# Optimization experiments

Hardware: AMD Instinct MI355X
Metric: run time of the kernel (lower is better)

## Reference

```python
import jax, jax.numpy as jnp
import numpy as np
import math

B, T, DIM, NH = 2, 2048, 2048, 16
HD = DIM // NH  # 128


def rotate_half(x):
    h = x.shape[-1] // 2
    return jnp.concatenate([-x[..., h:], x[..., :h]], axis=-1)


def rope_tables(t_len, rot_dim, base=10000.0, dtype=jnp.float32):
    # rot_dim = head_dim; inv_freq has rot_dim//2 entries -> sin/cos [T, rot_dim//2]
    inv_freq = 1.0 / (base ** (jnp.arange(0, rot_dim, 2, dtype=dtype) / rot_dim))
    t = jnp.arange(t_len, dtype=dtype)
    ang = jnp.einsum('i,j->ij', t, inv_freq)  # [T, rot_dim//2]
    return jnp.sin(ang), jnp.cos(ang)


def apply_rope(q, k, sin, cos):
    # Partial RoPE as in source: rotate only the first half of head_dim,
    # using sin/cos of width head_dim//2 matched to that half.
    h = q.shape[-1] // 2
    q1, q2 = q[..., :h], q[..., h:]
    k1, k2 = k[..., :h], k[..., h:]
    sin = sin[None, None]  # [1,1,T,h]
    cos = cos[None, None]
    q1r = q1 * cos + rotate_half(q1) * sin
    k1r = k1 * cos + rotate_half(k1) * sin
    return jnp.concatenate([q1r, q2], axis=-1), jnp.concatenate([k1r, k2], axis=-1)


def setup_inputs() -> dict:
    key = jax.random.key(0)
    ks = jax.random.split(key, 5)
    s = 1.0 / math.sqrt(DIM)
    return {
        'x': jax.random.normal(ks[0], (B, T, DIM), jnp.float32),
        'wq': jax.random.normal(ks[1], (DIM, DIM), jnp.float32) * s,
        'wk': jax.random.normal(ks[2], (DIM, DIM), jnp.float32) * s,
        'wv': jax.random.normal(ks[3], (DIM, DIM), jnp.float32) * s,
        'wo': jax.random.normal(ks[4], (DIM, DIM), jnp.float32) * s,
    }


def reference(x, wq, wk, wv, wo):
    b, t, c = x.shape
    def proj(w):
        return (x @ w.T).reshape(b, t, NH, HD).transpose(0, 2, 1, 3)  # [B,H,T,hd]
    q, k, v = proj(wq), proj(wk), proj(wv)
    sin, cos = rope_tables(t, HD, dtype=x.dtype)
    q, k = apply_rope(q, k, sin, cos)
    att = jnp.einsum('bhqd,bhkd->bhqk', q, k) * (1.0 / math.sqrt(HD))  # [B,H,T,T]
    att = jax.nn.softmax(att, axis=-1)
    y = jnp.einsum('bhqk,bhkd->bhqd', att, v)
    y = y.transpose(0, 2, 1, 3).reshape(b, t, c)
    return y @ wo.T
```

## Files before the change

kernel.cpp:

```cpp
#include <hip/hip_runtime.h>

typedef unsigned short u16;
typedef __attribute__((ext_vector_type(4))) u16 u16x4;
typedef __attribute__((ext_vector_type(8))) __bf16 bf16x8;
typedef __attribute__((ext_vector_type(4))) float f32x4;

#define B_ 2
#define T_ 2048
#define DIM_ 2048
#define NH_ 16
#define HD_ 128

__device__ __forceinline__ u16 f2b(float f) {
  unsigned u = __builtin_bit_cast(unsigned, f);
  u += 0x7fffu + ((u >> 16) & 1u);
  return (u16)(u >> 16);
}
__device__ __forceinline__ float b2f(u16 h) {
  unsigned u = ((unsigned)h) << 16;
  return __builtin_bit_cast(float, u);
}
__device__ __forceinline__ unsigned pack2(float lo, float hi) {
  return (unsigned)f2b(lo) | ((unsigned)f2b(hi) << 16);
}

typedef __attribute__((address_space(1))) void gvoid_t;
typedef __attribute__((address_space(3))) void lvoid_t;
__device__ __forceinline__ void gload16(const void* g, void* l) {
  __builtin_amdgcn_global_load_lds((gvoid_t*)g, (lvoid_t*)l, 16, 0, 0);
}

__global__ __launch_bounds__(256) void cvt_bf16(const float* x, const float* wq,
    const float* wk, const float* wv, const float* wo,
    u16* xb, u16* wqb, u16* wkb, u16* wvb, u16* wob) {
  int ten = blockIdx.y;
  const float* s; u16* d; int n4;
  if (ten == 0)      { s = x;  d = xb;  n4 = 2097152; }
  else if (ten == 1) { s = wq; d = wqb; n4 = 1048576; }
  else if (ten == 2) { s = wk; d = wkb; n4 = 1048576; }
  else if (ten == 3) { s = wv; d = wvb; n4 = 1048576; }
  else               { s = wo; d = wob; n4 = 1048576; }
  int i = blockIdx.x * 256 + threadIdx.x;
  if (i >= n4) return;
  float4 f = ((const float4*)s)[i];
  u16x4 o = { f2b(f.x), f2b(f.y), f2b(f.z), f2b(f.w) };
  ((u16x4*)d)[i] = o;
}

template <typename OutT>
__device__ __forceinline__ void gemm256_body(const u16* A, const u16* Bw, OutT* C) {
  constexpr int K = 2048, N = 2048;
  __shared__ u16 As[3][256 * 64];
  __shared__ u16 Bs[3][128 * 64];
  const int tid = threadIdx.x;
  const int w = tid >> 6, l = tid & 63, n = l & 15, quad = l >> 4;
  const int wr = w >> 1, wc = w & 1;
  const int row0 = blockIdx.y * 256, col0 = blockIdx.x * 128;

  const u16* aSrc[4];
  const u16* bSrc[2];
#pragma unroll
  for (int i = 0; i < 4; ++i) {
    int ci = i * 512 + tid, r = ci >> 3, cl = ci & 7, cg = cl ^ (r & 7);
    aSrc[i] = A + (size_t)(row0 + r) * K + cg * 8;
  }
#pragma unroll
  for (int i = 0; i < 2; ++i) {
    int ci = i * 512 + tid, r = ci >> 3, cl = ci & 7, cg = cl ^ (r & 7);
    bSrc[i] = Bw + (size_t)(col0 + r) * K + cg * 8;
  }
  const int ldsW = (w * 64) * 16;

  auto stA = [&](int kt, int bufi, int i) {
    gload16(aSrc[i] + kt * 64, (char*)As[bufi] + i * 8192 + ldsW);
  };
  auto stB = [&](int kt, int bufi, int i) {
    gload16(bSrc[i] + kt * 64, (char*)Bs[bufi] + i * 8192 + ldsW);
  };

  const int arow = (wr * 64 + n) * 64;
  const int brow = (wc * 64 + n) * 64;
  const int sw = n & 7;

  f32x4 acc[4][4] = {};

#pragma unroll
  for (int i = 0; i < 4; ++i) stA(0, 0, i);
#pragma unroll
  for (int i = 0; i < 2; ++i) stB(0, 0, i);
#pragma unroll
  for (int i = 0; i < 4; ++i) stA(1, 1, i);
#pragma unroll
  for (int i = 0; i < 2; ++i) stB(1, 1, i);
  asm volatile("s_waitcnt vmcnt(6)" ::: "memory");
  __builtin_amdgcn_s_barrier();

  int buf = 0, nbuf = 2;
#pragma unroll 1
  for (int kt = 0; kt < 32; ++kt) {
    const bool pf = kt < 30;
    const u16* Ab = As[buf];
    const u16* Bb = Bs[buf];
    bf16x8 af[4][2], bfr[2][2];

#pragma unroll
    for (int mt = 0; mt < 4; ++mt)
#pragma unroll
      for (int ks = 0; ks < 2; ++ks)
        af[mt][ks] = *(const bf16x8*)&Ab[arow + mt * 1024 + (((ks * 4 + quad) ^ sw) * 8)];
#pragma unroll
    for (int nt = 0; nt < 2; ++nt)
#pragma unroll
      for (int ks = 0; ks < 2; ++ks)
        bfr[nt][ks] = *(const bf16x8*)&Bb[brow + nt * 1024 + (((ks * 4 + quad) ^ sw) * 8)];
    if (pf) { stA(kt + 2, nbuf, 0); stA(kt + 2, nbuf, 1); stB(kt + 2, nbuf, 0); }
    __builtin_amdgcn_s_barrier();
    asm volatile("s_waitcnt lgkmcnt(0)" ::: "memory");
    __builtin_amdgcn_sched_barrier(0);
    __builtin_amdgcn_s_setprio(1);
#pragma unroll
    for (int ks = 0; ks < 2; ++ks)
#pragma unroll
      for (int mt = 0; mt < 4; ++mt)
#pragma unroll
        for (int nt = 0; nt < 2; ++nt)
          acc[mt][nt] = __builtin_amdgcn_mfma_f32_16x16x32_bf16(af[mt][ks], bfr[nt][ks], acc[mt][nt], 0, 0, 0);
    __builtin_amdgcn_s_setprio(0);
    __builtin_amdgcn_s_barrier();

#pragma unroll
    for (int nt = 0; nt < 2; ++nt)
#pragma unroll
      for (int ks = 0; ks < 2; ++ks)
        bfr[nt][ks] = *(const bf16x8*)&Bb[brow + (nt + 2) * 1024 + (((ks * 4 + quad) ^ sw) * 8)];
    if (pf) { stA(kt + 2, nbuf, 2); stA(kt + 2, nbuf, 3); stB(kt + 2, nbuf, 1); }
    if (pf) asm volatile("s_waitcnt vmcnt(6)" ::: "memory");
    else    asm volatile("s_waitcnt vmcnt(0)" ::: "memory");
    __builtin_amdgcn_s_barrier();
    asm volatile("s_waitcnt lgkmcnt(0)" ::: "memory");
    __builtin_amdgcn_sched_barrier(0);
    __builtin_amdgcn_s_setprio(1);
#pragma unroll
    for (int ks = 0; ks < 2; ++ks)
#pragma unroll
      for (int mt = 0; mt < 4; ++mt)
#pragma unroll
        for (int nt = 0; nt < 2; ++nt)
          acc[mt][nt + 2] = __builtin_amdgcn_mfma_f32_16x16x32_bf16(af[mt][ks], bfr[nt][ks], acc[mt][nt + 2], 0, 0, 0);
    __builtin_amdgcn_s_setprio(0);
    __builtin_amdgcn_s_barrier();

    buf = (buf == 2) ? 0 : buf + 1;
    nbuf = (nbuf == 2) ? 0 : nbuf + 1;
  }

#pragma unroll
  for (int mt = 0; mt < 4; ++mt)
#pragma unroll
    for (int nt = 0; nt < 4; ++nt)
#pragma unroll
      for (int r = 0; r < 4; ++r) {
        size_t idx = (size_t)(row0 + wr * 64 + mt * 16 + quad * 4 + r) * N + (col0 + wc * 64 + nt * 16 + n);
        float v = acc[mt][nt][r];
        if constexpr (sizeof(OutT) == 2) C[idx] = f2b(v); else C[idx] = v;
      }
}

__global__ __launch_bounds__(512, 2) void gemm_qkv(const u16* A, const u16* w0, const u16* w1,
    const u16* w2, u16* c0, u16* c1, u16* c2) {
  const u16* Bw = (blockIdx.z == 0) ? w0 : (blockIdx.z == 1) ? w1 : w2;
  u16* C = (blockIdx.z == 0) ? c0 : (blockIdx.z == 1) ? c1 : c2;
  gemm256_body<u16>(A, Bw, C);
}
__global__ __launch_bounds__(512, 2) void gemm_o(const u16* A, const u16* Bw, float* C) {
  gemm256_body<float>(A, Bw, C);
}

__global__ __launch_bounds__(256) void rope_k(u16* Qb, u16* Kb) {
  int gid = blockIdx.x * 256 + threadIdx.x;
  int j = gid & 31;
  int h = (gid >> 5) & 15;
  int row = gid >> 9;
  int t = row & (T_ - 1);
  bool isQ = (blockIdx.y == 0);
  u16* base = (isQ ? Qb : Kb) + (size_t)row * DIM_ + h * HD_;
  double f1 = exp2(-(double)j * 0.20762050593045951);
  double f2 = f1 * 0.01;
  const double INV2PI = 0.15915494309189535;
  double r1d = (double)t * f1 * INV2PI; r1d -= floor(r1d);
  double r2d = (double)t * f2 * INV2PI; r2d -= floor(r2d);
  float rv1 = (float)r1d, rv2 = (float)r2d;
  float c1 = __builtin_amdgcn_cosf(rv1), s1 = __builtin_amdgcn_sinf(rv1);
  float c2 = __builtin_amdgcn_cosf(rv2), s2 = __builtin_amdgcn_sinf(rv2);
  float x1 = b2f(base[j]), x2 = b2f(base[j + 32]);
  float scale = isQ ? 0.12751743342408354f : 1.0f;
  base[j]      = f2b((x1 * c1 - x2 * s1) * scale);
  base[j + 32] = f2b((x2 * c2 + x1 * s2) * scale);
  if (isQ) {
    base[j + 64] = f2b(b2f(base[j + 64]) * scale);
    base[j + 96] = f2b(b2f(base[j + 96]) * scale);
  }
}

__global__ __launch_bounds__(256) void transpose_v(const u16* V, u16* Vt) {
  int b = blockIdx.z;
  int t0 = blockIdx.x * 64, c0 = blockIdx.y * 64;
  __shared__ u16 tile[64][72];
  int tid = threadIdx.x;
#pragma unroll
  for (int i = 0; i < 4; ++i) {
    int v = i * 256 + tid;
    int r = v >> 4, c4 = (v & 15) * 4;
    *(u16x4*)&tile[r][c4] = *(const u16x4*)(V + (size_t)(b * T_ + t0 + r) * DIM_ + c0 + c4);
  }
  __syncthreads();
#pragma unroll
  for (int i = 0; i < 4; ++i) {
    int v = i * 256 + tid;
    int d = v >> 4, t4 = (v & 15) * 4;
    u16x4 o = { tile[t4 + 0][d], tile[t4 + 1][d], tile[t4 + 2][d], tile[t4 + 3][d] };
    *(u16x4*)(Vt + (size_t)(b * DIM_ + c0 + d) * T_ + t0 + t4) = o;
  }
}

__global__ __launch_bounds__(256, 2) void attn_k(const u16* Q, const u16* K, const u16* Vt, u16* Y) {
  const int qt = blockIdx.x, bh = blockIdx.y;
  const int b = bh >> 4, h = bh & 15;
  const int tid = threadIdx.x;
  const int w = tid >> 6, l = tid & 63, n = l & 15, quad = l >> 4;
  __shared__ u16 Ks[2][64 * 128];
  __shared__ u16 Vs[2][128 * 64];

  const u16* Qbase = Q + (size_t)(b * T_ + qt * 128 + w * 32) * DIM_ + h * HD_;
  const u16* Kbase = K + (size_t)(b * T_) * DIM_ + h * HD_;
  const u16* Vbase = Vt + (size_t)(b * DIM_ + h * HD_) * T_;

  bf16x8 qf[2][4];
#pragma unroll
  for (int qtile = 0; qtile < 2; ++qtile)
#pragma unroll
    for (int ks = 0; ks < 4; ++ks)
      qf[qtile][ks] = *(const bf16x8*)(Qbase + (size_t)(qtile * 16 + n) * DIM_ + ks * 32 + quad * 8);

  auto stageK = [&](int itn, u16* dst) {
#pragma unroll
    for (int inst = 0; inst < 4; ++inst) {
      int ci = inst * 256 + w * 64 + l;
      int r = ci >> 4, cl = ci & 15;
      int cg = cl ^ (r & 7);
      gload16(Kbase + (size_t)(itn * 64 + r) * DIM_ + cg * 8, (char*)dst + (inst * 256 + w * 64) * 16);
    }
  };
  auto stageV = [&](int itn, u16* dst) {
#pragma unroll
    for (int inst = 0; inst < 4; ++inst) {
      int ci = inst * 256 + w * 64 + l;
      int r = ci >> 3, cl = ci & 7;
      int cg = cl ^ (r & 7);
      gload16(Vbase + (size_t)r * T_ + itn * 64 + cg * 8, (char*)dst + (inst * 256 + w * 64) * 16);
    }
  };

  f32x4 o[2][8] = {};
  float m_r[2] = { -__builtin_inff(), -__builtin_inff() };
  float l_r[2] = { 0.f, 0.f };

  const int shA = ((quad & 1) * 2) * 16 + n;
  const int shB = shA + 16;
  const bool hiTile = (quad >= 2);

  auto iter_body = [&](const u16* Kc, const u16* Vc, u16* Kn, u16* Vn, int itn) {
    __syncthreads();
    if (itn >= 0) { stageK(itn, Kn); stageV(itn, Vn); }

    f32x4 st[2][4] = {};
#pragma unroll
    for (int ks = 0; ks < 4; ++ks) {
      bf16x8 kf[4];
#pragma unroll
      for (int mt = 0; mt < 4; ++mt)
        kf[mt] = *(const bf16x8*)&Kc[(mt * 16 + n) * 128 + (((ks * 4 + quad) ^ (n & 7)) * 8)];
#pragma unroll
      for (int qtile = 0; qtile < 2; ++qtile)
#pragma unroll
        for (int mt = 0; mt < 4; ++mt)
          st[qtile][mt] = __builtin_amdgcn_mfma_f32_16x16x32_bf16(kf[mt], qf[qtile][ks], st[qtile][mt], 0, 0, 0);
    }

    unsigned pk[2][4][2];
#pragma unroll
    for (int qtile = 0; qtile < 2; ++qtile) {
      float mx = -__builtin_inff();
#pragma unroll
      for (int mt = 0; mt < 4; ++mt)
#pragma unroll
        for (int r = 0; r < 4; ++r) mx = fmaxf(mx, st[qtile][mt][r]);
      mx = fmaxf(mx, __shfl_xor(mx, 16, 64));
      mx = fmaxf(mx, __shfl_xor(mx, 32, 64));
      float mo = m_r[qtile];
      float mn = fmaxf(mo, mx);
      float al = __builtin_amdgcn_exp2f(mo - mn);
      float rs = 0.f;
#pragma unroll
      for (int mt = 0; mt < 4; ++mt)
#pragma unroll
        for (int r = 0; r < 4; ++r) {
          float p = __builtin_amdgcn_exp2f(st[qtile][mt][r] - mn);
          st[qtile][mt][r] = p;
          rs += p;
        }
      rs += __shfl_xor(rs, 16, 64);
      rs += __shfl_xor(rs, 32, 64);
      l_r[qtile] = al * l_r[qtile] + rs;
      m_r[qtile] = mn;
#pragma unroll
      for (int mt = 0; mt < 4; ++mt) {
        pk[qtile][mt][0] = pack2(st[qtile][mt][0], st[qtile][mt][1]);
        pk[qtile][mt][1] = pack2(st[qtile][mt][2], st[qtile][mt][3]);
      }
#pragma unroll
      for (int mt = 0; mt < 8; ++mt)
#pragma unroll
        for (int r = 0; r < 4; ++r) o[qtile][mt][r] *= al;
    }

    typedef __attribute__((ext_vector_type(4))) unsigned uint4v;
    uint4v pT[2][2];
#pragma unroll
    for (int qtile = 0; qtile < 2; ++qtile)
#pragma unroll
      for (int ks2 = 0; ks2 < 2; ++ks2)
#pragma unroll
        for (int jj = 0; jj < 4; ++jj) {
          int src = (jj < 2) ? shA : shB;
          unsigned vA = __shfl((int)pk[qtile][ks2 * 2][jj & 1], src, 64);
          unsigned vB = __shfl((int)pk[qtile][ks2 * 2 + 1][jj & 1], src, 64);
          pT[qtile][ks2][jj] = hiTile ? vB : vA;
        }

#pragma unroll
    for (int ks2 = 0; ks2 < 2; ++ks2) {
      bf16x8 vf[8];
#pragma unroll
      for (int mt = 0; mt < 8; ++mt)
        vf[mt] = *(const bf16x8*)&Vc[(mt * 16 + n) * 64 + (((ks2 * 4 + quad) ^ (n & 7)) * 8)];
#pragma unroll
      for (int qtile = 0; qtile < 2; ++qtile) {
        bf16x8 pfrag = __builtin_bit_cast(bf16x8, pT[qtile][ks2]);
#pragma unroll
        for (int mt = 0; mt < 8; ++mt)
          o[qtile][mt] = __builtin_amdgcn_mfma_f32_16x16x32_bf16(vf[mt], pfrag, o[qtile][mt], 0, 0, 0);
      }
    }
  };

  stageK(0, Ks[0]); stageV(0, Vs[0]);
  for (int it = 0; it < 32; it += 2) {
    iter_body(Ks[0], Vs[0], Ks[1], Vs[1], it + 1);
    iter_body(Ks[1], Vs[1], Ks[0], Vs[0], (it + 2 < 32) ? it + 2 : -1);
  }

  u16* Ybase = Y + (size_t)(b * T_ + qt * 128 + w * 32) * DIM_ + h * HD_;
#pragma unroll
  for (int qtile = 0; qtile < 2; ++qtile) {
    float inv = 1.0f / l_r[qtile];
#pragma unroll
    for (int mt = 0; mt < 8; ++mt) {
      u16x4 ov = { f2b(o[qtile][mt][0] * inv), f2b(o[qtile][mt][1] * inv),
                   f2b(o[qtile][mt][2] * inv), f2b(o[qtile][mt][3] * inv) };
      *(u16x4*)(Ybase + (size_t)(qtile * 16 + n) * DIM_ + mt * 16 + quad * 4) = ov;
    }
  }
}

extern "C" void kernel_launch(void* const* d_in, const int* in_sizes, int n_in,
                              void* d_out, int out_size, void* d_ws, size_t ws_size,
                              hipStream_t stream) {
  const float* x  = (const float*)d_in[0];
  const float* wq = (const float*)d_in[1];
  const float* wk = (const float*)d_in[2];
  const float* wv = (const float*)d_in[3];
  const float* wo = (const float*)d_in[4];

  u16* ws  = (u16*)d_ws;
  u16* xb  = ws;
  u16* wqb = xb + 8388608;
  u16* wkb = wqb + 4194304;
  u16* wvb = wkb + 4194304;
  u16* wob = wvb + 4194304;
  u16* qb  = wob + 4194304;
  u16* kb  = qb + 8388608;
  u16* vb  = kb + 8388608;
  u16* vt  = vb + 8388608;
  u16* yb  = vt + 8388608;

  cvt_bf16<<<dim3(8192, 5), 256, 0, stream>>>(x, wq, wk, wv, wo, xb, wqb, wkb, wvb, wob);
  gemm_qkv<<<dim3(16, 16, 3), 512, 0, stream>>>(xb, wqb, wkb, wvb, qb, kb, vb);
  rope_k<<<dim3(8192, 2), 256, 0, stream>>>(qb, kb);
  transpose_v<<<dim3(32, 32, 2), 256, 0, stream>>>(vb, vt);
  attn_k<<<dim3(16, 32), 256, 0, stream>>>(qb, kb, vt, yb);
  gemm_o<<<dim3(16, 16), 512, 0, stream>>>(yb, wob, (float*)d_out);
}
```

Measured before the change: 405.2 us.

## Use K=32 triple-buffered GEMM body for QKV with higher occupancy; flatten convert grid

The QKV projection GEMM gets a new body with 32-wide K tiles and a three-stage LDS ring. Prefetch is issued two tiles ahead inside an unrolled-by-3 loop with partial vmcnt waits, and launch bounds are raised to 4 blocks per CU. The smaller LDS footprint is meant to allow more resident blocks and better latency hiding, at the cost of more barriers per K step. The bf16 conversion kernel is also flattened to a 1D grid so no idle blocks are launched for the smaller weight tensors.

New measurement: 408.6 us. Within noise of the previous version (+0.8%).

```diff
diff --git a/kernel.cpp b/kernel.cpp
--- a/kernel.cpp
+++ b/kernel.cpp
@@ -33,18 +33,114 @@
 __global__ __launch_bounds__(256) void cvt_bf16(const float* x, const float* wq,
     const float* wk, const float* wv, const float* wo,
     u16* xb, u16* wqb, u16* wkb, u16* wvb, u16* wob) {
-  int ten = blockIdx.y;
-  const float* s; u16* d; int n4;
-  if (ten == 0)      { s = x;  d = xb;  n4 = 2097152; }
-  else if (ten == 1) { s = wq; d = wqb; n4 = 1048576; }
-  else if (ten == 2) { s = wk; d = wkb; n4 = 1048576; }
-  else if (ten == 3) { s = wv; d = wvb; n4 = 1048576; }
-  else               { s = wo; d = wob; n4 = 1048576; }
   int i = blockIdx.x * 256 + threadIdx.x;
-  if (i >= n4) return;
-  float4 f = ((const float4*)s)[i];
+  const float* s; u16* d; int off;
+  if (i < 2097152) { s = x; d = xb; off = i; }
+  else {
+    int j = i - 2097152, t = j >> 20;
+    off = j & 1048575;
+    if (t == 0)      { s = wq; d = wqb; }
+    else if (t == 1) { s = wk; d = wkb; }
+    else if (t == 2) { s = wv; d = wvb; }
+    else             { s = wo; d = wob; }
+  }
+  float4 f = ((const float4*)s)[off];
   u16x4 o = { f2b(f.x), f2b(f.y), f2b(f.z), f2b(f.w) };
-  ((u16x4*)d)[i] = o;
+  ((u16x4*)d)[off] = o;
+}
+
+template <typename OutT>
+__device__ __forceinline__ void gemm3r_body(const u16* A, const u16* Bw, OutT* C) {
+  constexpr int K = 2048, N = 2048;
+  __shared__ u16 As3[3][256 * 32];
+  __shared__ u16 Bs3[3][128 * 32];
+  const int tid = threadIdx.x;
+  const int w = tid >> 6, l = tid & 63, n = l & 15, quad = l >> 4;
+  const int wr = w >> 1, wc = w & 1;
+  const int row0 = blockIdx.y * 256, col0 = blockIdx.x * 128;
+
+  const u16* aS0; const u16* aS1; const u16* bS;
+  {
+    int r = tid >> 2, cl = tid & 3, cg = cl ^ ((r >> 1) & 3);
+    aS0 = A + (size_t)(row0 + r) * K + cg * 8;
+    bS  = Bw + (size_t)(col0 + r) * K + cg * 8;
+    int ci2 = 512 + tid, r2 = ci2 >> 2, cg2 = (ci2 & 3) ^ ((r2 >> 1) & 3);
+    aS1 = A + (size_t)(row0 + r2) * K + cg2 * 8;
+  }
+  const int ldsW = w * 1024;
+
+  auto stA = [&](int kt, u16* dst) {
+    gload16(aS0 + kt * 32, (char*)dst + ldsW);
+    gload16(aS1 + kt * 32, (char*)dst + 8192 + ldsW);
+  };
+  auto stB = [&](int kt, u16* dst) {
+    gload16(bS + kt * 32, (char*)dst + ldsW);
+  };
+
+  const int pos = (quad ^ ((n >> 1) & 3)) * 8;
+  const int aRd = (wr * 64 + n) * 32 + pos;
+  const int bRd = (wc * 64 + n) * 32 + pos;
+
+  f32x4 acc[4][4] = {};
+
+  u16 *A0 = As3[0], *A1 = As3[1], *A2 = As3[2];
+  u16 *B0 = Bs3[0], *B1 = Bs3[1], *B2 = Bs3[2];
+
+  stA(0, A0); stB(0, B0);
+  stA(1, A1); stB(1, B1);
+  asm volatile("s_waitcnt vmcnt(3)" ::: "memory");
+  __builtin_amdgcn_s_barrier();
+  asm volatile("" ::: "memory");
+
+  auto ktile = [&](int kt, const u16* Ac, const u16* Bc, u16* Asg, u16* Bsg, int mode) {
+    bf16x8 bfr[4], af[4];
+#pragma unroll
+    for (int nt = 0; nt < 4; ++nt)
+      bfr[nt] = *(const bf16x8*)(Bc + bRd + nt * 512);
+#pragma unroll
+    for (int mt = 0; mt < 4; ++mt)
+      af[mt] = *(const bf16x8*)(Ac + aRd + mt * 512);
+    if (mode == 0) { stA(kt + 2, Asg); stB(kt + 2, Bsg); }
+    __builtin_amdgcn_s_setprio(1);
+#pragma unroll
+    for (int mt = 0; mt < 4; ++mt)
+#pragma unroll
+      for (int nt = 0; nt < 4; ++nt)
+        acc[mt][nt] = __builtin_amdgcn_mfma_f32_16x16x32_bf16(af[mt], bfr[nt], acc[mt][nt], 0, 0, 0);
+    __builtin_amdgcn_s_setprio(0);
+    if (mode == 0)      asm volatile("s_waitcnt vmcnt(3)" ::: "memory");
+    else if (mode == 1) asm volatile("s_waitcnt vmcnt(0)" ::: "memory");
+    if (mode <= 1) { __builtin_amdgcn_s_barrier(); asm volatile("" ::: "memory"); }
+  };
+
+#pragma unroll 1
+  for (int kt = 0; kt < 60; kt += 3) {
+    ktile(kt + 0, A0, B0, A2, B2, 0);
+    ktile(kt + 1, A1, B1, A0, B0, 0);
+    ktile(kt + 2, A2, B2, A1, B1, 0);
+  }
+  ktile(60, A0, B0, A2, B2, 0);
+  ktile(61, A1, B1, A0, B0, 0);
+  ktile(62, A2, B2, A1, B1, 1);
+  ktile(63, A0, B0, A1, B1, 2);
+
+#pragma unroll
+  for (int mt = 0; mt < 4; ++mt)
+#pragma unroll
+    for (int nt = 0; nt < 4; ++nt)
+#pragma unroll
+      for (int r = 0; r < 4; ++r) {
+        size_t idx = (size_t)(row0 + wr * 64 + mt * 16 + quad * 4 + r) * N + (col0 + wc * 64 + nt * 16 + n);
+        float v = acc[mt][nt][r];
+        if constexpr (sizeof(OutT) == 2) C[idx] = f2b(v); else C[idx] = v;
+      }
+}
+
+__global__ __launch_bounds__(512, 4) void gemm_qkv(const u16* A, const u16* w0, const u16* w1,
+    const u16* w2, u16* c0, u16* c1, u16* c2) {
+  const u16* Bw = (blockIdx.z == 0) ? w0 : (blockIdx.z == 1) ? w1 : w2;
+  u16* C = (blockIdx.z == 0) ? c0 : (blockIdx.z == 1) ? c1 : c2;
+  gemm3r_body<u16>(A, Bw, C);
 }
 
 template <typename OutT>
@@ -166,12 +262,6 @@
       }
 }
 
-__global__ __launch_bounds__(512, 2) void gemm_qkv(const u16* A, const u16* w0, const u16* w1,
-    const u16* w2, u16* c0, u16* c1, u16* c2) {
-  const u16* Bw = (blockIdx.z == 0) ? w0 : (blockIdx.z == 1) ? w1 : w2;
-  u16* C = (blockIdx.z == 0) ? c0 : (blockIdx.z == 1) ? c1 : c2;
-  gemm256_body<u16>(A, Bw, C);
-}
 __global__ __launch_bounds__(512, 2) void gemm_o(const u16* A, const u16* Bw, float* C) {
   gemm256_body<float>(A, Bw, C);
 }
@@ -394,7 +484,7 @@
   u16* vt  = vb + 8388608;
   u16* yb  = vt + 8388608;
 
-  cvt_bf16<<<dim3(8192, 5), 256, 0, stream>>>(x, wq, wk, wv, wo, xb, wqb, wkb, wvb, wob);
+  cvt_bf16<<<dim3(24576), 256, 0, stream>>>(x, wq, wk, wv, wo, xb, wqb, wkb, wvb, wob);
   gemm_qkv<<<dim3(16, 16, 3), 512, 0, stream>>>(xb, wqb, wkb, wvb, qb, kb, vb);
   rope_k<<<dim3(8192, 2), 256, 0, stream>>>(qb, kb);
   transpose_v<<<dim3(32, 32, 2), 256, 0, stream>>>(vb, vt);
```
